# Kernel tuning notes

Measured on AMD Instinct MI355X. Metric: run time of the kernel, lower is better.

The kernel has to match this reference:

```python
import jax, jax.numpy as jnp
import numpy as np
from jax import lax

PATCH = 17
THRESH = 0.5


def _bbox_from_mask(mask_np):
    # mask_np: [D,H,W] bool. Matches mask_to_3d_bbox (min/max of nonzero coords).
    z, y, x = np.nonzero(mask_np)
    return (int(x.min()), int(y.min()), int(z.min()),
            int(x.max()), int(y.max()), int(z.max()))


def _extract_patches(vol, bbox):
    # vol: [1,1,D,H,W]; crop uses exclusive max (slice z_min:z_max) like the torch code
    x0, y0, z0, x1, y1, z1 = bbox
    t = vol[:, :, z0:z1, y0:y1, x0:x1]
    pads = []
    for d in t.shape[2:]:
        r = d % PATCH
        p = (PATCH - r) % PATCH
        pads.append((p // 2, p - p // 2))
    t = jnp.pad(t, ((0, 0), (0, 0), pads[0], pads[1], pads[2]))
    D, H, W = t.shape[2:]
    nD, nH, nW = D // PATCH, H // PATCH, W // PATCH
    p = t.reshape(nD, PATCH, nH, PATCH, nW, PATCH)
    p = p.transpose(0, 2, 4, 1, 3, 5).reshape(-1, PATCH, PATCH, PATCH)
    return p[:, None]  # [N,1,17,17,17]


def _conv3d(x, w, b, stride):
    y = lax.conv_general_dilated(x, w, (stride,) * 3, 'VALID',
                                 dimension_numbers=('NCDHW', 'OIDHW', 'NCDHW'))
    return y + b.reshape(1, -1, 1, 1, 1)


def _model(fixed, moving, c1w, c1b, c2w, c2b, f1w, f1b, f2w, f2b):
    # Stand-in for the opaque torch.jit model: siamese-concat 3D CNN -> MLP -> tanh.
    x = jnp.concatenate([fixed, moving], axis=1)          # [N,2,17,17,17]
    x = jax.nn.relu(_conv3d(x, c1w, c1b, 2))              # [N,32,8,8,8]
    x = jax.nn.relu(_conv3d(x, c2w, c2b, 2))              # [N,64,3,3,3]
    x = x.reshape(x.shape[0], -1)                         # [N,1728]
    x = jax.nn.relu(x @ f1w.T + f1b)                      # [N,256]
    return jnp.tanh(x @ f2w.T + f2b)                      # [N,1]


def setup_inputs() -> dict:
    key = jax.random.key(0)
    ks = jax.random.split(key, 10)
    V = 222
    source = jax.random.normal(ks[0], (1, 1, V, V, V), jnp.float32)
    target = jax.random.uniform(ks[1], (1, 1, V, V, V), jnp.float32)
    fc_in = 64 * 3 * 3 * 3
    return {
        'source': source,
        'target': target,
        'conv1_w': jax.random.normal(ks[2], (32, 2, 3, 3, 3), jnp.float32) * 0.1,
        'conv1_b': jnp.zeros((32,), jnp.float32),
        'conv2_w': jax.random.normal(ks[3], (64, 32, 3, 3, 3), jnp.float32) * 0.05,
        'conv2_b': jnp.zeros((64,), jnp.float32),
        'fc1_w': jax.random.normal(ks[4], (256, fc_in), jnp.float32) * 0.02,
        'fc1_b': jnp.zeros((256,), jnp.float32),
        'fc2_w': jax.random.normal(ks[5], (1, 256), jnp.float32) * 0.05,
        'fc2_b': jnp.zeros((1,), jnp.float32),
    }


def reference(source, target, conv1_w, conv1_b, conv2_w, conv2_b,
              fc1_w, fc1_b, fc2_w, fc2_b):
    mask_np = np.asarray(target) > 0
    bbox = _bbox_from_mask(mask_np.squeeze())
    fixed_patches = _extract_patches(target, bbox)   # [N,1,17,17,17]
    moving_patches = _extract_patches(source, bbox)
    # per-patch zero fraction on fixed patches; keep if <= threshold
    zero_frac = jnp.mean((fixed_patches[:, 0] == 0).astype(jnp.float32), axis=(1, 2, 3))
    keep = (zero_frac <= THRESH).astype(jnp.float32)  # [N]
    out = _model(fixed_patches, moving_patches, conv1_w, conv1_b, conv2_w, conv2_b,
                 fc1_w, fc1_b, fc2_w, fc2_b)          # [N,1]
    # mean over kept patches == weighted mean (stream-compaction-free, same math)
    return jnp.sum(out[:, 0] * keep) / jnp.sum(keep)
```

## Files before the change

kernel.cpp:

```cpp
#include <hip/hip_runtime.h>


static constexpr int kPS = 433;
static constexpr int kRS = 25;
static constexpr int kCS = 528;
static constexpr int kZS = 66;
static constexpr int kHOff = 6912;

template <bool PACKED>
static __device__ __forceinline__ float2 dmr16_patch(
    int p, int t,
    const float* __restrict__ src, const float* __restrict__ tgt,
    const float* __restrict__ c1w, const float* __restrict__ c1b,
    const float* __restrict__ c2w, const float* __restrict__ c2b,
    const float* __restrict__ fw,  const float* __restrict__ f1b,
    const float* __restrict__ f2w, const float* __restrict__ f2b,
    float* __restrict__ sBuf, float* __restrict__ sRed) {
  int pd = p / 169; int rem = p - pd * 169; int phh = rem / 13; int pww = rem - phh * 13;
  int z0 = pd * 17, y0 = phh * 17, x0 = pww * 17;

  int wv  = t >> 6;
  int od  = (t >> 3) & 7, oh = t & 7;
  int oc2 = t & 63;

  float cnt = 0.f;
  for (int idx = t; idx < 4913; idx += 256) {
    int a = idx / 289; int r2 = idx - a * 289; int b = r2 / 17; int c = r2 - b * 17;
    float v = tgt[((size_t)(z0 + a) * 222 + (y0 + b)) * 222 + (x0 + c)];
    sBuf[a * kPS + b * kRS + c] = v;
    if (v == 0.0f) cnt += 1.f;
  }
  sRed[t] = cnt;
  __syncthreads();
  for (int o = 128; o > 0; o >>= 1) {
    if (t < o) sRed[t] += sRed[t + o];
    __syncthreads();
  }
  float keep = (sRed[0] / 4913.0f <= 0.5f) ? 1.0f : 0.0f;
  __syncthreads();

  float acc2[27];
  #pragma unroll
  for (int i = 0; i < 27; i++) acc2[i] = 0.f;

  #pragma unroll 1
  for (int half = 0; half < 2; half++) {
    float acc[4][8];
    #pragma unroll
    for (int i = 0; i < 4; i++)
      #pragma unroll
      for (int j = 0; j < 8; j++) acc[i][j] = 0.f;

    #pragma unroll 1
    for (int ic = 0; ic < 2; ic++) {
      if (half + ic > 0) {
        const float* vol = ic ? src : tgt;
        __syncthreads();
        for (int idx = t; idx < 4913; idx += 256) {
          int a = idx / 289; int r2 = idx - a * 289; int b = r2 / 17; int c = r2 - b * 17;
          sBuf[a * kPS + b * kRS + c] =
              vol[((size_t)(z0 + a) * 222 + (y0 + b)) * 222 + (x0 + c)];
        }
        __syncthreads();
      }
      #pragma unroll 1
      for (int td = 0; td < 3; td++) {
        #pragma unroll 1
        for (int th = 0; th < 3; th++) {
          int rbase = (2 * od + td) * kPS + (2 * oh + th) * kRS;
          float a[17];
          #pragma unroll
          for (int x = 0; x < 17; x++) a[x] = sBuf[rbase + x];
          #pragma unroll
          for (int ocr = 0; ocr < 4; ocr++) {
            int oc = half * 16 + wv * 4 + ocr;
            const float* wp = c1w + oc * 54 + ic * 27 + td * 9 + th * 3;
            float w0 = wp[0], w1 = wp[1], w2 = wp[2];
            #pragma unroll
            for (int ow = 0; ow < 8; ow++)
              acc[ocr][ow] += a[2 * ow] * w0 + a[2 * ow + 1] * w1 + a[2 * ow + 2] * w2;
          }
        }
      }
    }
    __syncthreads();
    #pragma unroll
    for (int ocr = 0; ocr < 4; ocr++) {
      int lo = wv * 4 + ocr;
      float b = c1b[half * 16 + lo];
      int base = lo * kCS + od * kZS + oh * 8;
      #pragma unroll
      for (int ow = 0; ow < 8; ow++)
        sBuf[base + ow] = fmaxf(acc[ocr][ow] + b, 0.f);
    }
    __syncthreads();

    #pragma unroll 1
    for (int icr = 0; icr < 4; icr++) {
      int icl = wv * 4 + icr;
      int ic  = half * 16 + icl;
      const float* cbase = sBuf + icl * kCS;
      #pragma unroll 1
      for (int td = 0; td < 3; td++) {
        #pragma unroll 1
        for (int th = 0; th < 3; th++) {
          const float* wp = c2w + oc2 * 864 + ic * 27 + td * 9 + th * 3;
          float w0 = wp[0], w1 = wp[1], w2 = wp[2];
          #pragma unroll
          for (int zo = 0; zo < 3; zo++) {
            #pragma unroll
            for (int yo = 0; yo < 3; yo++) {
              const float* rp = cbase + (2 * zo + td) * kZS + (2 * yo + th) * 8;
              #pragma unroll
              for (int xo = 0; xo < 3; xo++)
                acc2[zo * 9 + yo * 3 + xo] +=
                    rp[2 * xo] * w0 + rp[2 * xo + 1] * w1 + rp[2 * xo + 2] * w2;
            }
          }
        }
      }
    }
  }
  __syncthreads();
  #pragma unroll
  for (int pos = 0; pos < 27; pos++)
    sBuf[(wv * 27 + pos) * 64 + oc2] = acc2[pos];
  __syncthreads();
  float* sH = sBuf + kHOff;
  for (int idx = t; idx < 1728; idx += 256) {
    int o = idx & 63, pos = idx >> 6;
    float v = sBuf[pos * 64 + o] + sBuf[(27 + pos) * 64 + o] +
              sBuf[(54 + pos) * 64 + o] + sBuf[(81 + pos) * 64 + o];
    sH[o * 27 + pos] = fmaxf(v + c2b[o], 0.f);
  }
  __syncthreads();

  float acc1 = 0.f;
  if (PACKED) {
    const float4* w4p = (const float4*)fw;
    const float4* sH4 = (const float4*)sH;
    #pragma unroll 8
    for (int k4 = 0; k4 < 432; k4++) {
      float4 w  = w4p[k4 * 256 + t];
      float4 hv = sH4[k4];
      acc1 += w.x * hv.x + w.y * hv.y + w.z * hv.z + w.w * hv.w;
    }
  } else {
    const float* frow = fw + (size_t)t * 1728;
    #pragma unroll 8
    for (int k = 0; k < 1728; k++) acc1 += sH[k] * frow[k];
  }
  float h = fmaxf(acc1 + f1b[t], 0.f);
  sRed[t] = h * f2w[t];
  __syncthreads();
  for (int o = 128; o > 0; o >>= 1) {
    if (t < o) sRed[t] += sRed[t + o];
    __syncthreads();
  }
  float2 rk;
  rk.x = tanhf(sRed[0] + f2b[0]) * keep;
  rk.y = keep;
  __syncthreads();
  return rk;
}

__global__ void dmr16_tr(const float* __restrict__ f1w, float* __restrict__ w1t4) {
  int k4 = blockIdx.x;
  int n  = threadIdx.x;
  const float* s = f1w + (size_t)n * 1728 + k4 * 4;
  float4 w;
  w.x = s[0]; w.y = s[1]; w.z = s[2]; w.w = s[3];
  ((float4*)w1t4)[k4 * 256 + n] = w;
}

__global__ __launch_bounds__(256, 4)
void DMMRLoss_52621939310662_kernel(
    const float* __restrict__ src, const float* __restrict__ tgt,
    const float* __restrict__ c1w, const float* __restrict__ c1b,
    const float* __restrict__ c2w, const float* __restrict__ c2b,
    const float* __restrict__ w1t4, const float* __restrict__ f1b,
    const float* __restrict__ f2w, const float* __restrict__ f2b,
    float* __restrict__ pr, float* __restrict__ pk) {
  __shared__ float sBuf[8704];
  __shared__ float sRed[256];
  int t = threadIdx.x;
  float2 rk = dmr16_patch<true>(blockIdx.x, t, src, tgt, c1w, c1b, c2w, c2b,
                                w1t4, f1b, f2w, f2b, sBuf, sRed);
  if (t == 0) { pr[blockIdx.x] = rk.x; pk[blockIdx.x] = rk.y; }
}

__global__ __launch_bounds__(256, 4)
void dmr16_hot_raw(const float* __restrict__ src, const float* __restrict__ tgt,
                   const float* __restrict__ c1w, const float* __restrict__ c1b,
                   const float* __restrict__ c2w, const float* __restrict__ c2b,
                   const float* __restrict__ f1w, const float* __restrict__ f1b,
                   const float* __restrict__ f2w, const float* __restrict__ f2b,
                   float* __restrict__ pr, float* __restrict__ pk) {
  __shared__ float sBuf[8704];
  __shared__ float sRed[256];
  int t = threadIdx.x;
  float2 rk = dmr16_patch<false>(blockIdx.x, t, src, tgt, c1w, c1b, c2w, c2b,
                                 f1w, f1b, f2w, f2b, sBuf, sRed);
  if (t == 0) { pr[blockIdx.x] = rk.x; pk[blockIdx.x] = rk.y; }
}

__global__ void dmr16_reduce(const float* __restrict__ pr, const float* __restrict__ pk,
                             float* __restrict__ out) {
  __shared__ float s1[256], s2[256];
  int t = threadIdx.x;
  float a = 0.f, b = 0.f;
  for (int p = t; p < 2197; p += 256) { a += pr[p]; b += pk[p]; }
  s1[t] = a; s2[t] = b;
  __syncthreads();
  for (int o = 128; o > 0; o >>= 1) {
    if (t < o) { s1[t] += s1[t + o]; s2[t] += s2[t + o]; }
    __syncthreads();
  }
  if (t == 0) out[0] = s1[0] / s2[0];
}

__global__ __launch_bounds__(256, 4)
void dmr16_solo(const float* __restrict__ src, const float* __restrict__ tgt,
                const float* __restrict__ c1w, const float* __restrict__ c1b,
                const float* __restrict__ c2w, const float* __restrict__ c2b,
                const float* __restrict__ f1w, const float* __restrict__ f1b,
                const float* __restrict__ f2w, const float* __restrict__ f2b,
                float* __restrict__ out) {
  __shared__ float sBuf[8704];
  __shared__ float sRed[256];
  __shared__ float sAcc[2];
  int t = threadIdx.x;
  if (t == 0) { sAcc[0] = 0.f; sAcc[1] = 0.f; }
  for (int p = 0; p < 2197; p++) {
    __syncthreads();
    float2 rk = dmr16_patch<false>(p, t, src, tgt, c1w, c1b, c2w, c2b,
                                   f1w, f1b, f2w, f2b, sBuf, sRed);
    if (t == 0) { sAcc[0] += rk.x; sAcc[1] += rk.y; }
  }
  __syncthreads();
  if (t == 0) out[0] = sAcc[0] / sAcc[1];
}

extern "C" void kernel_launch(void* const* d_in, const int* in_sizes, int n_in,
                              void* d_out, int out_size, void* d_ws, size_t ws_size,
                              hipStream_t stream) {
  const float* src = (const float*)d_in[0];
  const float* tgt = (const float*)d_in[1];
  const float* c1w = (const float*)d_in[2];
  const float* c1b = (const float*)d_in[3];
  const float* c2w = (const float*)d_in[4];
  const float* c2b = (const float*)d_in[5];
  const float* f1w = (const float*)d_in[6];
  const float* f1b = (const float*)d_in[7];
  const float* f2w = (const float*)d_in[8];
  const float* f2b = (const float*)d_in[9];
  float* out = (float*)d_out;

  const size_t nW1T = 442368;
  const size_t nPK  = 2 * 2197;
  if (d_ws && ws_size >= (nW1T + nPK) * sizeof(float)) {
    float* w1t4 = (float*)d_ws;
    float* pr   = w1t4 + nW1T;
    float* pk   = pr + 2197;
    dmr16_tr<<<432, 256, 0, stream>>>(f1w, w1t4);
    DMMRLoss_52621939310662_kernel<<<2197, 256, 0, stream>>>(
        src, tgt, c1w, c1b, c2w, c2b, w1t4, f1b, f2w, f2b, pr, pk);
    dmr16_reduce<<<1, 256, 0, stream>>>(pr, pk, out);
  } else if (d_ws && ws_size >= nPK * sizeof(float)) {
    float* pr = (float*)d_ws;
    float* pk = pr + 2197;
    dmr16_hot_raw<<<2197, 256, 0, stream>>>(
        src, tgt, c1w, c1b, c2w, c2b, f1w, f1b, f2w, f2b, pr, pk);
    dmr16_reduce<<<1, 256, 0, stream>>>(pr, pk, out);
  } else {
    dmr16_solo<<<1, 256, 0, stream>>>(
        src, tgt, c1w, c1b, c2w, c2b, f1w, f1b, f2w, f2b, out);
  }
}
```

Measured before the change: 437.8 us.

## Split FC1 out of per-patch kernel into a batched tiled GEMM

```diff
diff --git a/kernel.cpp b/kernel.cpp
--- a/kernel.cpp
+++ b/kernel.cpp
@@ -5,17 +5,17 @@
 static constexpr int kRS = 25;
 static constexpr int kCS = 528;
 static constexpr int kZS = 66;
-static constexpr int kHOff = 6912;
-
-template <bool PACKED>
-static __device__ __forceinline__ float2 dmr16_patch(
-    int p, int t,
+
+__global__ __launch_bounds__(256, 4)
+void DMMRLoss_52621939310662_kernel(
     const float* __restrict__ src, const float* __restrict__ tgt,
     const float* __restrict__ c1w, const float* __restrict__ c1b,
     const float* __restrict__ c2w, const float* __restrict__ c2b,
-    const float* __restrict__ fw,  const float* __restrict__ f1b,
-    const float* __restrict__ f2w, const float* __restrict__ f2b,
-    float* __restrict__ sBuf, float* __restrict__ sRed) {
+    float* __restrict__ h2, float* __restrict__ pk) {
+  __shared__ float sBuf[8704];
+  __shared__ float sRed[256];
+  int p = blockIdx.x;
+  int t = threadIdx.x;
   int pd = p / 169; int rem = p - pd * 169; int phh = rem / 13; int pww = rem - phh * 13;
   int z0 = pd * 17, y0 = phh * 17, x0 = pww * 17;
 
@@ -37,6 +37,7 @@
     __syncthreads();
   }
   float keep = (sRed[0] / 4913.0f <= 0.5f) ? 1.0f : 0.0f;
+  if (t == 0) pk[p] = keep;
   __syncthreads();
 
   float acc2[27];
@@ -126,90 +127,102 @@
   for (int pos = 0; pos < 27; pos++)
     sBuf[(wv * 27 + pos) * 64 + oc2] = acc2[pos];
   __syncthreads();
-  float* sH = sBuf + kHOff;
+  float* h2p = h2 + (size_t)p * 1728;
   for (int idx = t; idx < 1728; idx += 256) {
     int o = idx & 63, pos = idx >> 6;
     float v = sBuf[pos * 64 + o] + sBuf[(27 + pos) * 64 + o] +
               sBuf[(54 + pos) * 64 + o] + sBuf[(81 + pos) * 64 + o];
-    sH[o * 27 + pos] = fmaxf(v + c2b[o], 0.f);
-  }
-  __syncthreads();
-
-  float acc1 = 0.f;
-  if (PACKED) {
-    const float4* w4p = (const float4*)fw;
-    const float4* sH4 = (const float4*)sH;
-    #pragma unroll 8
-    for (int k4 = 0; k4 < 432; k4++) {
-      float4 w  = w4p[k4 * 256 + t];
-      float4 hv = sH4[k4];
-      acc1 += w.x * hv.x + w.y * hv.y + w.z * hv.z + w.w * hv.w;
-    }
-  } else {
-    const float* frow = fw + (size_t)t * 1728;
-    #pragma unroll 8
-    for (int k = 0; k < 1728; k++) acc1 += sH[k] * frow[k];
-  }
-  float h = fmaxf(acc1 + f1b[t], 0.f);
-  sRed[t] = h * f2w[t];
-  __syncthreads();
-  for (int o = 128; o > 0; o >>= 1) {
-    if (t < o) sRed[t] += sRed[t + o];
-    __syncthreads();
-  }
-  float2 rk;
-  rk.x = tanhf(sRed[0] + f2b[0]) * keep;
-  rk.y = keep;
-  __syncthreads();
-  return rk;
-}
-
-__global__ void dmr16_tr(const float* __restrict__ f1w, float* __restrict__ w1t4) {
+    h2p[idx] = fmaxf(v + c2b[o], 0.f);
+  }
+}
+
+__global__ void dmr22_pack(const float* __restrict__ f1w, float* __restrict__ wp4) {
   int k4 = blockIdx.x;
   int n  = threadIdx.x;
-  const float* s = f1w + (size_t)n * 1728 + k4 * 4;
   float4 w;
-  w.x = s[0]; w.y = s[1]; w.z = s[2]; w.w = s[3];
-  ((float4*)w1t4)[k4 * 256 + n] = w;
-}
+  float* pw = (float*)&w;
+  #pragma unroll
+  for (int j = 0; j < 4; j++) {
+    int kp = k4 * 4 + j;
+    int o = kp & 63, pos = kp >> 6;
+    pw[j] = f1w[(size_t)n * 1728 + (o * 27 + pos)];
+  }
+  ((float4*)wp4)[(size_t)k4 * 256 + n] = w;
+}
+
+static constexpr int kKT = 192;
+static constexpr int kTS = 36;
 
 __global__ __launch_bounds__(256, 4)
-void DMMRLoss_52621939310662_kernel(
-    const float* __restrict__ src, const float* __restrict__ tgt,
-    const float* __restrict__ c1w, const float* __restrict__ c1b,
-    const float* __restrict__ c2w, const float* __restrict__ c2b,
-    const float* __restrict__ w1t4, const float* __restrict__ f1b,
-    const float* __restrict__ f2w, const float* __restrict__ f2b,
-    float* __restrict__ pr, float* __restrict__ pk) {
-  __shared__ float sBuf[8704];
-  __shared__ float sRed[256];
+void dmr22_gemm(const float* __restrict__ h2, const float* __restrict__ wp4,
+                const float* __restrict__ f1b, const float* __restrict__ f2w,
+                float* __restrict__ part) {
+  __shared__ float sT[kKT * kTS];
+  int b = blockIdx.x;
+  int pg = b >> 2, ng = b & 3;
+  int p0 = pg * 32;
   int t = threadIdx.x;
-  float2 rk = dmr16_patch<true>(blockIdx.x, t, src, tgt, c1w, c1b, c2w, c2b,
-                                w1t4, f1b, f2w, f2b, sBuf, sRed);
-  if (t == 0) { pr[blockIdx.x] = rk.x; pk[blockIdx.x] = rk.y; }
-}
-
-__global__ __launch_bounds__(256, 4)
-void dmr16_hot_raw(const float* __restrict__ src, const float* __restrict__ tgt,
-                   const float* __restrict__ c1w, const float* __restrict__ c1b,
-                   const float* __restrict__ c2w, const float* __restrict__ c2b,
-                   const float* __restrict__ f1w, const float* __restrict__ f1b,
-                   const float* __restrict__ f2w, const float* __restrict__ f2b,
-                   float* __restrict__ pr, float* __restrict__ pk) {
-  __shared__ float sBuf[8704];
-  __shared__ float sRed[256];
-  int t = threadIdx.x;
-  float2 rk = dmr16_patch<false>(blockIdx.x, t, src, tgt, c1w, c1b, c2w, c2b,
-                                 f1w, f1b, f2w, f2b, sBuf, sRed);
-  if (t == 0) { pr[blockIdx.x] = rk.x; pk[blockIdx.x] = rk.y; }
-}
-
-__global__ void dmr16_reduce(const float* __restrict__ pr, const float* __restrict__ pk,
-                             float* __restrict__ out) {
+  int n = ng * 64 + (t & 63);
+  int pgrp = t >> 6;
+
+  float acc[8];
+  #pragma unroll
+  for (int i = 0; i < 8; i++) acc[i] = 0.f;
+
+  #pragma unroll 1
+  for (int kt = 0; kt < 1728; kt += kKT) {
+    __syncthreads();
+    #pragma unroll 1
+    for (int i = 0; i < (32 * kKT) / 256; i++) {
+      int idx = i * 256 + t;
+      int pp = idx / kKT, kk = idx - pp * kKT;
+      sT[kk * kTS + pp] = h2[(size_t)(p0 + pp) * 1728 + kt + kk];
+    }
+    __syncthreads();
+    #pragma unroll 2
+    for (int k4 = 0; k4 < kKT / 4; k4++) {
+      float4 w = ((const float4*)wp4)[(size_t)((kt >> 2) + k4) * 256 + n];
+      const float* r0 = sT + (k4 * 4 + 0) * kTS + pgrp * 8;
+      const float* r1 = sT + (k4 * 4 + 1) * kTS + pgrp * 8;
+      const float* r2 = sT + (k4 * 4 + 2) * kTS + pgrp * 8;
+      const float* r3 = sT + (k4 * 4 + 3) * kTS + pgrp * 8;
+      float4 a0 = *(const float4*)r0, b0 = *(const float4*)(r0 + 4);
+      float4 a1 = *(const float4*)r1, b1 = *(const float4*)(r1 + 4);
+      float4 a2 = *(const float4*)r2, b2 = *(const float4*)(r2 + 4);
+      float4 a3 = *(const float4*)r3, b3 = *(const float4*)(r3 + 4);
+      acc[0] += w.x * a0.x + w.y * a1.x + w.z * a2.x + w.w * a3.x;
+      acc[1] += w.x * a0.y + w.y * a1.y + w.z * a2.y + w.w * a3.y;
+      acc[2] += w.x * a0.z + w.y * a1.z + w.z * a2.z + w.w * a3.z;
+      acc[3] += w.x * a0.w + w.y * a1.w + w.z * a2.w + w.w * a3.w;
+      acc[4] += w.x * b0.x + w.y * b1.x + w.z * b2.x + w.w * b3.x;
+      acc[5] += w.x * b0.y + w.y * b1.y + w.z * b2.y + w.w * b3.y;
+      acc[6] += w.x * b0.z + w.y * b1.z + w.z * b2.z + w.w * b3.z;
+      acc[7] += w.x * b0.w + w.y * b1.w + w.z * b2.w + w.w * b3.w;
+    }
+  }
+  float b1v = f1b[n], w2v = f2w[n];
+  #pragma unroll
+  for (int pp = 0; pp < 8; pp++) {
+    float tl = fmaxf(acc[pp] + b1v, 0.f) * w2v;
+    #pragma unroll
+    for (int o = 32; o > 0; o >>= 1) tl += __shfl_down(tl, o, 64);
+    if ((t & 63) == 0)
+      part[(size_t)(p0 + pgrp * 8 + pp) * 4 + ng] = tl;
+  }
+}
+
+__global__ void dmr22_fin(const float* __restrict__ part, const float* __restrict__ pk,
+                          const float* __restrict__ f2b, float* __restrict__ out) {
   __shared__ float s1[256], s2[256];
   int t = threadIdx.x;
+  float b0 = f2b[0];
   float a = 0.f, b = 0.f;
-  for (int p = t; p < 2197; p += 256) { a += pr[p]; b += pk[p]; }
+  for (int p = t; p < 2197; p += 256) {
+    float s = part[4 * p] + part[4 * p + 1] + part[4 * p + 2] + part[4 * p + 3];
+    float kv = pk[p];
+    a += tanhf(s + b0) * kv;
+    b += kv;
+  }
   s1[t] = a; s2[t] = b;
   __syncthreads();
   for (int o = 128; o > 0; o >>= 1) {
@@ -219,23 +232,142 @@
   if (t == 0) out[0] = s1[0] / s2[0];
 }
 
-__global__ __launch_bounds__(256, 4)
-void dmr16_solo(const float* __restrict__ src, const float* __restrict__ tgt,
+__global__ __launch_bounds__(256, 2)
+void dmr22_solo(const float* __restrict__ src, const float* __restrict__ tgt,
                 const float* __restrict__ c1w, const float* __restrict__ c1b,
                 const float* __restrict__ c2w, const float* __restrict__ c2b,
                 const float* __restrict__ f1w, const float* __restrict__ f1b,
                 const float* __restrict__ f2w, const float* __restrict__ f2b,
                 float* __restrict__ out) {
   __shared__ float sBuf[8704];
+  __shared__ float sH[1728];
   __shared__ float sRed[256];
   __shared__ float sAcc[2];
   int t = threadIdx.x;
+  int wv = t >> 6, od = (t >> 3) & 7, oh = t & 7, oc2 = t & 63;
   if (t == 0) { sAcc[0] = 0.f; sAcc[1] = 0.f; }
   for (int p = 0; p < 2197; p++) {
     __syncthreads();
-    float2 rk = dmr16_patch<false>(p, t, src, tgt, c1w, c1b, c2w, c2b,
-                                   f1w, f1b, f2w, f2b, sBuf, sRed);
-    if (t == 0) { sAcc[0] += rk.x; sAcc[1] += rk.y; }
+    int pd = p / 169; int rem = p - pd * 169; int phh = rem / 13; int pww = rem - phh * 13;
+    int z0 = pd * 17, y0 = phh * 17, x0 = pww * 17;
+    float cnt = 0.f;
+    for (int idx = t; idx < 4913; idx += 256) {
+      int a = idx / 289; int r2 = idx - a * 289; int b = r2 / 17; int c = r2 - b * 17;
+      float v = tgt[((size_t)(z0 + a) * 222 + (y0 + b)) * 222 + (x0 + c)];
+      sBuf[a * kPS + b * kRS + c] = v;
+      if (v == 0.0f) cnt += 1.f;
+    }
+    sRed[t] = cnt;
+    __syncthreads();
+    for (int o = 128; o > 0; o >>= 1) {
+      if (t < o) sRed[t] += sRed[t + o];
+      __syncthreads();
+    }
+    float keep = (sRed[0] / 4913.0f <= 0.5f) ? 1.0f : 0.0f;
+    __syncthreads();
+    float acc2[27];
+    for (int i = 0; i < 27; i++) acc2[i] = 0.f;
+    #pragma unroll 1
+    for (int half = 0; half < 2; half++) {
+      float acc[4][8];
+      for (int i = 0; i < 4; i++)
+        for (int j = 0; j < 8; j++) acc[i][j] = 0.f;
+      #pragma unroll 1
+      for (int ic = 0; ic < 2; ic++) {
+        if (half + ic > 0) {
+          const float* vol = ic ? src : tgt;
+          __syncthreads();
+          for (int idx = t; idx < 4913; idx += 256) {
+            int a = idx / 289; int r2 = idx - a * 289; int b = r2 / 17; int c = r2 - b * 17;
+            sBuf[a * kPS + b * kRS + c] =
+                vol[((size_t)(z0 + a) * 222 + (y0 + b)) * 222 + (x0 + c)];
+          }
+          __syncthreads();
+        }
+        #pragma unroll 1
+        for (int td = 0; td < 3; td++) {
+          #pragma unroll 1
+          for (int th = 0; th < 3; th++) {
+            int rbase = (2 * od + td) * kPS + (2 * oh + th) * kRS;
+            float a[17];
+            #pragma unroll
+            for (int x = 0; x < 17; x++) a[x] = sBuf[rbase + x];
+            #pragma unroll
+            for (int ocr = 0; ocr < 4; ocr++) {
+              int oc = half * 16 + wv * 4 + ocr;
+              const float* wp = c1w + oc * 54 + ic * 27 + td * 9 + th * 3;
+              float w0 = wp[0], w1 = wp[1], w2 = wp[2];
+              #pragma unroll
+              for (int ow = 0; ow < 8; ow++)
+                acc[ocr][ow] += a[2 * ow] * w0 + a[2 * ow + 1] * w1 + a[2 * ow + 2] * w2;
+            }
+          }
+        }
+      }
+      __syncthreads();
+      #pragma unroll
+      for (int ocr = 0; ocr < 4; ocr++) {
+        int lo = wv * 4 + ocr;
+        float b = c1b[half * 16 + lo];
+        int base = lo * kCS + od * kZS + oh * 8;
+        #pragma unroll
+        for (int ow = 0; ow < 8; ow++)
+          sBuf[base + ow] = fmaxf(acc[ocr][ow] + b, 0.f);
+      }
+      __syncthreads();
+      #pragma unroll 1
+      for (int icr = 0; icr < 4; icr++) {
+        int icl = wv * 4 + icr;
+        int ic  = half * 16 + icl;
+        const float* cbase = sBuf + icl * kCS;
+        #pragma unroll 1
+        for (int td = 0; td < 3; td++) {
+          #pragma unroll 1
+          for (int th = 0; th < 3; th++) {
+            const float* wp = c2w + oc2 * 864 + ic * 27 + td * 9 + th * 3;
+            float w0 = wp[0], w1 = wp[1], w2 = wp[2];
+            #pragma unroll
+            for (int zo = 0; zo < 3; zo++) {
+              #pragma unroll
+              for (int yo = 0; yo < 3; yo++) {
+                const float* rp = cbase + (2 * zo + td) * kZS + (2 * yo + th) * 8;
+                #pragma unroll
+                for (int xo = 0; xo < 3; xo++)
+                  acc2[zo * 9 + yo * 3 + xo] +=
+                      rp[2 * xo] * w0 + rp[2 * xo + 1] * w1 + rp[2 * xo + 2] * w2;
+              }
+            }
+          }
+        }
+      }
+    }
+    __syncthreads();
+    #pragma unroll
+    for (int pos = 0; pos < 27; pos++)
+      sBuf[(wv * 27 + pos) * 64 + oc2] = acc2[pos];
+    __syncthreads();
+    for (int idx = t; idx < 1728; idx += 256) {
+      int o = idx & 63, pos = idx >> 6;
+      float v = sBuf[pos * 64 + o] + sBuf[(27 + pos) * 64 + o] +
+                sBuf[(54 + pos) * 64 + o] + sBuf[(81 + pos) * 64 + o];
+      sH[o * 27 + pos] = fmaxf(v + c2b[o], 0.f);
+    }
+    __syncthreads();
+    float acc1 = 0.f;
+    const float* frow = f1w + (size_t)t * 1728;
+    #pragma unroll 8
+    for (int k = 0; k < 1728; k++) acc1 += sH[k] * frow[k];
+    float h = fmaxf(acc1 + f1b[t], 0.f);
+    sRed[t] = h * f2w[t];
+    __syncthreads();
+    for (int o = 128; o > 0; o >>= 1) {
+      if (t < o) sRed[t] += sRed[t + o];
+      __syncthreads();
+    }
+    if (t == 0) {
+      sAcc[0] += tanhf(sRed[0] + f2b[0]) * keep;
+      sAcc[1] += keep;
+    }
   }
   __syncthreads();
   if (t == 0) out[0] = sAcc[0] / sAcc[1];
@@ -256,24 +388,22 @@
   const float* f2b = (const float*)d_in[9];
   float* out = (float*)d_out;
 
-  const size_t nW1T = 442368;
-  const size_t nPK  = 2 * 2197;
-  if (d_ws && ws_size >= (nW1T + nPK) * sizeof(float)) {
-    float* w1t4 = (float*)d_ws;
-    float* pr   = w1t4 + nW1T;
-    float* pk   = pr + 2197;
-    dmr16_tr<<<432, 256, 0, stream>>>(f1w, w1t4);
+  const size_t nWP  = 442368;
+  const size_t nH2  = (size_t)2208 * 1728;
+  const size_t nPart = 2208 * 4;
+  const size_t nPk  = 2208;
+  if (d_ws && ws_size >= (nWP + nH2 + nPart + nPk) * sizeof(float)) {
+    float* wp4  = (float*)d_ws;
+    float* h2   = wp4 + nWP;
+    float* part = h2 + nH2;
+    float* pk   = part + nPart;
+    dmr22_pack<<<432, 256, 0, stream>>>(f1w, wp4);
     DMMRLoss_52621939310662_kernel<<<2197, 256, 0, stream>>>(
-        src, tgt, c1w, c1b, c2w, c2b, w1t4, f1b, f2w, f2b, pr, pk);
-    dmr16_reduce<<<1, 256, 0, stream>>>(pr, pk, out);
-  } else if (d_ws && ws_size >= nPK * sizeof(float)) {
-    float* pr = (float*)d_ws;
-    float* pk = pr + 2197;
-    dmr16_hot_raw<<<2197, 256, 0, stream>>>(
-        src, tgt, c1w, c1b, c2w, c2b, f1w, f1b, f2w, f2b, pr, pk);
-    dmr16_reduce<<<1, 256, 0, stream>>>(pr, pk, out);
+        src, tgt, c1w, c1b, c2w, c2b, h2, pk);
+    dmr22_gemm<<<276, 256, 0, stream>>>(h2, wp4, f1b, f2w, part);
+    dmr22_fin<<<1, 256, 0, stream>>>(part, pk, f2b, out);
   } else {
-    dmr16_solo<<<1, 256, 0, stream>>>(
+    dmr22_solo<<<1, 256, 0, stream>>>(
         src, tgt, c1w, c1b, c2w, c2b, f1w, f1b, f2w, f2b, out);
   }
 }
```

New measurement: 441.0 us. No clear change (+0.7%).
